# Kernel optimization log

Measured on AMD Instinct MI355X. Metric: run time of the kernel, lower is better.

Reference implementation:

```python
import jax, jax.numpy as jnp
import numpy as np

B, T, D = 1024, 512, 128  # batch, history length, embedding = num_units


def setup_inputs() -> dict:
    key = jax.random.key(0)
    ks = jax.random.split(key, 5)
    s = 1.0 / np.sqrt(2 * D)
    return {
        "rnn_input": jax.random.normal(ks[0], (B, T, D), jnp.float32),
        "att_score": jax.random.uniform(ks[1], (B, T, 1), jnp.float32),
        "gate_kernel": jax.random.normal(ks[2], (2 * D, 2 * D), jnp.float32) * s,
        "gate_bias": jnp.ones((2 * D,), jnp.float32),  # TF GRUCell init: gate bias = 1.0
        "cand_kernel": jax.random.normal(ks[3], (2 * D, D), jnp.float32) * s,
        "cand_bias": jnp.zeros((D,), jnp.float32),
        "sequence_length": jax.random.randint(ks[4], (B, 1), 1, T + 1, jnp.int32),
    }


def reference(rnn_input, att_score, gate_kernel, gate_bias, cand_kernel, cand_bias, sequence_length):
    # AUGRU (VecAttGRUCell) dynamic_rnn, return_sequence=True
    Bv, Tv, Dv = rnn_input.shape
    lens = sequence_length.reshape(Bv)                      # tf.squeeze
    x_t = jnp.transpose(rnn_input, (1, 0, 2))               # [T,B,D]
    a_t = jnp.transpose(att_score, (1, 0, 2))               # [T,B,1]
    mask = (jnp.arange(Tv)[:, None] < lens[None, :])[..., None]  # [T,B,1] bool
    h0 = jnp.zeros((Bv, Dv), rnn_input.dtype)

    def step(h, xs):
        x, a, m = xs
        gi = jnp.concatenate([x, h], -1) @ gate_kernel + gate_bias
        r, u = jnp.split(jax.nn.sigmoid(gi), 2, axis=-1)
        c = jnp.tanh(jnp.concatenate([x, r * h], -1) @ cand_kernel + cand_bias)
        u = (1.0 - a) * u                                   # attention-gated update
        new_h = u * h + (1.0 - u) * c
        h_next = jnp.where(m, new_h, h)                     # state copy-through past length
        out = jnp.where(m, new_h, 0.0)                      # dynamic_rnn zeros past length
        return h_next, out

    _, outs = jax.lax.scan(step, h0, (x_t, a_t, mask))
    return jnp.transpose(outs, (1, 0, 2))                   # [B,T,D]
```

## Files before the change

kernel.cpp:

```cpp
#include <hip/hip_runtime.h>
#include <hip/hip_bf16.h>


#define Bn 1024
#define Tn 512
#define Dn 128

typedef __attribute__((ext_vector_type(8))) short short8;
typedef __attribute__((ext_vector_type(4))) float f32x4;

#define BS 136

#define NL2E  (-1.4426950408889634f)
#define N2L2E (-2.8853900817779268f)

__device__ __forceinline__ short f2bf(float f) {
    __hip_bfloat16 h = __float2bfloat16(f);
    return __builtin_bit_cast(short, h);
}
__device__ __forceinline__ unsigned cvt_pk_bf16(float a, float b) {
    unsigned r;
    asm("v_cvt_pk_bf16_f32 %0, %1, %2" : "=v"(r) : "v"(a), "v"(b));
    return r;
}
__device__ __forceinline__ void barrier_lds() {
    __builtin_amdgcn_sched_barrier(0);
    asm volatile("s_waitcnt lgkmcnt(0)" ::: "memory");
    __builtin_amdgcn_s_barrier();
    __builtin_amdgcn_sched_barrier(0);
}

#define MFMA_(a, b, c) __builtin_amdgcn_mfma_f32_16x16x32_bf16((a), (b), (c), 0, 0, 0)

__launch_bounds__(512, 1)
__global__ void augru_kernel(const float* __restrict__ X,
                             const float* __restrict__ ATT,
                             const float* __restrict__ GK,
                             const float* __restrict__ GB,
                             const float* __restrict__ CK,
                             const float* __restrict__ CB,
                             const int*   __restrict__ SL,
                             float* __restrict__ OUT) {
    __shared__ short hb [16 * BS];
    __shared__ short rhb[16 * BS];
    __shared__ short xb [2][16 * BS];
    __shared__ float abuf[2][16];
    __shared__ int   lenbuf[16];

    const int tid  = threadIdx.x;
    const int wid  = tid >> 6;
    const int lane = tid & 63;
    const int lm   = lane & 15;
    const int q    = lane >> 4;
    const int b0   = blockIdx.x * 16;
    const int ccol = 16 * wid + lm;

    short8 fgx0[4], fgx1[4], fgh0[4], fgh1[4], fcx[4], fch[4];
#pragma unroll
    for (int ks = 0; ks < 4; ++ks) {
        short8 v0, v1, v2, v3, v4, v5;
#pragma unroll
        for (int j = 0; j < 8; ++j) {
            const int k = ks * 32 + q * 8 + j;
            v0[j] = f2bf(GK[k * 256 + ccol]);
            v1[j] = f2bf(GK[k * 256 + 128 + ccol]);
            v2[j] = f2bf(GK[(128 + k) * 256 + ccol]);
            v3[j] = f2bf(GK[(128 + k) * 256 + 128 + ccol]);
            v4[j] = f2bf(CK[k * 128 + ccol]);
            v5[j] = f2bf(CK[(128 + k) * 128 + ccol]);
        }
        fgx0[ks] = v0; fgx1[ks] = v1; fgh0[ks] = v2; fgh1[ks] = v3;
        fcx[ks] = v4;  fch[ks] = v5;
    }
    const float pb0 = GB[ccol]       * NL2E;
    const float pb1 = GB[128 + ccol] * NL2E;
    const float cbp = CB[ccol]       * N2L2E;

    for (int i = tid; i < 16 * BS; i += 512) hb[i] = 0;
    if (tid < 16) {
        lenbuf[tid]  = SL[b0 + tid];
        abuf[0][tid] = ATT[(size_t)(b0 + tid) * Tn];
    }
    const int prow = tid >> 5;
    const int pcol = (tid & 31) * 4;
    {
        float4 v = *(const float4*)(X + ((size_t)(b0 + prow) * Tn + 0) * Dn + pcol);
        uint2 pp; pp.x = cvt_pk_bf16(v.x, v.y); pp.y = cvt_pk_bf16(v.z, v.w);
        *(uint2*)&xb[0][prow * BS + pcol] = pp;
    }
    __syncthreads();

    int len_i[4];
    float h_reg[4] = {0.f, 0.f, 0.f, 0.f};
#pragma unroll
    for (int i = 0; i < 4; ++i) len_i[i] = lenbuf[q * 4 + i];

    f32x4 gxA0 = {0,0,0,0}, gxA1 = {0,0,0,0}, cxA = {0,0,0,0};
    f32x4 gxB0, gxB1, cxB;
    {
        short8 ax0[4];
#pragma unroll
        for (int ks = 0; ks < 4; ++ks)
            ax0[ks] = *(const short8*)&xb[0][lm * BS + ks * 32 + q * 8];
#pragma unroll
        for (int ks = 0; ks < 4; ++ks) {
            gxA0 = MFMA_(ax0[ks], fgx0[ks], gxA0);
            gxA1 = MFMA_(ax0[ks], fgx1[ks], gxA1);
            cxA  = MFMA_(ax0[ks], fcx[ks],  cxA);
        }
        float4 v = *(const float4*)(X + ((size_t)(b0 + prow) * Tn + 1) * Dn + pcol);
        uint2 pp; pp.x = cvt_pk_bf16(v.x, v.y); pp.y = cvt_pk_bf16(v.z, v.w);
        *(uint2*)&xb[1][prow * BS + pcol] = pp;
    }
    __syncthreads();

#define STEP_BODY(t, GIN0, GIN1, CIN, GOUT0, GOUT1, COUT)                         \
    {                                                                             \
        const int cur = (t) & 1, nxt = cur ^ 1;                                   \
        const int tp1 = ((t) + 1 < Tn) ? (t) + 1 : Tn - 1;                        \
        const int tp2 = ((t) + 2 < Tn) ? (t) + 2 : Tn - 1;                        \
        float4 xpre = *(const float4*)(X + ((size_t)(b0 + prow) * Tn + tp2) * Dn + pcol); \
        float  apre = (tid < 16) ? ATT[(size_t)(b0 + tid) * Tn + tp1] : 0.0f;     \
                                  \
        short8 axn[4], ah[4];                                                     \
        _Pragma("unroll")                                                         \
        for (int ks = 0; ks < 4; ++ks) {                                          \
            axn[ks] = *(const short8*)&xb[nxt][lm * BS + ks * 32 + q * 8];        \
            ah[ks]  = *(const short8*)&hb[lm * BS + ks * 32 + q * 8];             \
        }                                                                         \
         \
        f32x4 g0 = GIN0, g1 = GIN1;                                               \
        f32x4 n0 = {0,0,0,0}, n1 = {0,0,0,0}, n2 = {0,0,0,0};                     \
        _Pragma("unroll")                                                         \
        for (int ks = 0; ks < 4; ++ks) {                                          \
            g0 = MFMA_(ah[ks], fgh0[ks], g0);                                     \
            g1 = MFMA_(ah[ks], fgh1[ks], g1);                                     \
        }                                                                         \
        _Pragma("unroll")                                                         \
        for (int ks = 0; ks < 4; ++ks) {                                          \
            n0 = MFMA_(axn[ks], fgx0[ks], n0);                                    \
            n1 = MFMA_(axn[ks], fgx1[ks], n1);                                    \
            n2 = MFMA_(axn[ks], fcx[ks],  n2);                                    \
        }                                                                         \
              \
        float am[4], up[4], rhv[4];                                               \
        _Pragma("unroll")                                                         \
        for (int i = 0; i < 4; ++i) am[i] = 1.0f - abuf[cur][q * 4 + i];          \
        _Pragma("unroll")                                                         \
        for (int i = 0; i < 4; ++i) {                                             \
            const float e0 = __builtin_amdgcn_exp2f(fmaf(g0[i], NL2E, pb0));      \
            rhv[i] = __builtin_amdgcn_rcpf(1.0f + e0) * h_reg[i];                 \
            const float e1 = __builtin_amdgcn_exp2f(fmaf(g1[i], NL2E, pb1));      \
            up[i] = am[i] * __builtin_amdgcn_rcpf(1.0f + e1);                     \
        }                                                                         \
        {                                                                         \
            const unsigned pA_ = cvt_pk_bf16(rhv[0], rhv[1]);                     \
            const unsigned pB_ = cvt_pk_bf16(rhv[2], rhv[3]);                     \
            rhb[(q * 4 + 0) * BS + ccol] = (short)pA_;                            \
            rhb[(q * 4 + 1) * BS + ccol] = (short)(pA_ >> 16);                    \
            rhb[(q * 4 + 2) * BS + ccol] = (short)pB_;                            \
            rhb[(q * 4 + 3) * BS + ccol] = (short)(pB_ >> 16);                    \
        }                                                                         \
        barrier_lds();                                                            \
                               \
        f32x4 cc = CIN;                                                           \
        _Pragma("unroll")                                                         \
        for (int ks = 0; ks < 4; ++ks) {                                          \
            short8 arh = *(const short8*)&rhb[lm * BS + ks * 32 + q * 8];         \
            cc = MFMA_(arh, fch[ks], cc);                                         \
        }                                                                         \
                             \
        float hxv[4];                                                             \
        _Pragma("unroll")                                                         \
        for (int i = 0; i < 4; ++i) {                                             \
            const int row = q * 4 + i;                                            \
            const float e  = __builtin_amdgcn_exp2f(fmaf(cc[i], N2L2E, cbp));     \
            const float cv = fmaf(2.0f, __builtin_amdgcn_rcpf(1.0f + e), -1.0f);  \
            const float hn = fmaf(up[i], h_reg[i] - cv, cv);                      \
            const bool valid = ((t) < len_i[i]);                                  \
            const float hnext = valid ? hn : h_reg[i];                            \
            OUT[((size_t)(b0 + row) * Tn + (t)) * Dn + ccol] = valid ? hn : 0.0f; \
            h_reg[i] = hnext;                                                     \
            hxv[i] = hnext;                                                       \
        }                                                                         \
        {                                                                         \
            const unsigned pA_ = cvt_pk_bf16(hxv[0], hxv[1]);                     \
            const unsigned pB_ = cvt_pk_bf16(hxv[2], hxv[3]);                     \
            hb[(q * 4 + 0) * BS + ccol] = (short)pA_;                             \
            hb[(q * 4 + 1) * BS + ccol] = (short)(pA_ >> 16);                     \
            hb[(q * 4 + 2) * BS + ccol] = (short)pB_;                             \
            hb[(q * 4 + 3) * BS + ccol] = (short)(pB_ >> 16);                     \
        }                                                                         \
                            \
        {                                                                         \
            uint2 pp_;                                                            \
            pp_.x = cvt_pk_bf16(xpre.x, xpre.y);                                  \
            pp_.y = cvt_pk_bf16(xpre.z, xpre.w);                                  \
            *(uint2*)&xb[cur][prow * BS + pcol] = pp_;                            \
            if (tid < 16) abuf[nxt][tid] = apre;                                  \
        }                                                                         \
        barrier_lds();                                                            \
        GOUT0 = n0; GOUT1 = n1; COUT = n2;                                        \
    }

    for (int t = 0; t < Tn; t += 2) {
        STEP_BODY(t,     gxA0, gxA1, cxA, gxB0, gxB1, cxB)
        STEP_BODY(t + 1, gxB0, gxB1, cxB, gxA0, gxA1, cxA)
    }
#undef STEP_BODY
}

extern "C" void kernel_launch(void* const* d_in, const int* in_sizes, int n_in,
                              void* d_out, int out_size, void* d_ws, size_t ws_size,
                              hipStream_t stream) {
    (void)in_sizes; (void)n_in; (void)d_ws; (void)ws_size; (void)out_size;
    const float* X   = (const float*)d_in[0];
    const float* ATT = (const float*)d_in[1];
    const float* GK  = (const float*)d_in[2];
    const float* GB  = (const float*)d_in[3];
    const float* CK  = (const float*)d_in[4];
    const float* CB  = (const float*)d_in[5];
    const int*   SL  = (const int*)d_in[6];
    float* OUT = (float*)d_out;

    augru_kernel<<<dim3(Bn / 16), dim3(512), 0, stream>>>(X, ATT, GK, GB, CK, CB, SL, OUT);
}
```

Baseline: 526.6 us.

## Halve waves per block, giving each wave two column tiles of the GRU step

Each block now runs 4 waves instead of 8, and each wave computes two 16-column slices. It holds twice the bf16 weight fragments in registers and interleaves two independent MFMA accumulation chains. This is meant to cut barrier participants and improve MFMA issue overlap within a wave. The cost is a longer serial per-wave MFMA and transcendental sequence per timestep and much higher register pressure. X staging now uses 8-wide loads per thread, and the staged x for the next step is re-read inside a macro rather than taken from the early prefetch registers. That may expose global load latency unless the compiler merges the duplicate loads.

```diff
diff --git a/kernel.cpp b/kernel.cpp
--- a/kernel.cpp
+++ b/kernel.cpp
@@ -8,6 +8,7 @@
 
 typedef __attribute__((ext_vector_type(8))) short short8;
 typedef __attribute__((ext_vector_type(4))) float f32x4;
+typedef __attribute__((ext_vector_type(4))) unsigned uint4v;
 
 #define BS 136
 
@@ -32,7 +33,7 @@
 
 #define MFMA_(a, b, c) __builtin_amdgcn_mfma_f32_16x16x32_bf16((a), (b), (c), 0, 0, 0)
 
-__launch_bounds__(512, 1)
+__launch_bounds__(256, 1)
 __global__ void augru_kernel(const float* __restrict__ X,
                              const float* __restrict__ ATT,
                              const float* __restrict__ GK,
@@ -53,64 +54,77 @@
     const int lm   = lane & 15;
     const int q    = lane >> 4;
     const int b0   = blockIdx.x * 16;
-    const int ccol = 16 * wid + lm;
-
-    short8 fgx0[4], fgx1[4], fgh0[4], fgh1[4], fcx[4], fch[4];
-#pragma unroll
-    for (int ks = 0; ks < 4; ++ks) {
-        short8 v0, v1, v2, v3, v4, v5;
-#pragma unroll
-        for (int j = 0; j < 8; ++j) {
-            const int k = ks * 32 + q * 8 + j;
-            v0[j] = f2bf(GK[k * 256 + ccol]);
-            v1[j] = f2bf(GK[k * 256 + 128 + ccol]);
-            v2[j] = f2bf(GK[(128 + k) * 256 + ccol]);
-            v3[j] = f2bf(GK[(128 + k) * 256 + 128 + ccol]);
-            v4[j] = f2bf(CK[k * 128 + ccol]);
-            v5[j] = f2bf(CK[(128 + k) * 128 + ccol]);
+
+    const int colBase = 32 * wid + lm;
+
+    short8 fgx0[2][4], fgx1[2][4], fgh0[2][4], fgh1[2][4], fcx[2][4], fch[2][4];
+    float pb0[2], pb1[2], cbp[2];
+#pragma unroll
+    for (int s = 0; s < 2; ++s) {
+        const int c = colBase + 16 * s;
+#pragma unroll
+        for (int ks = 0; ks < 4; ++ks) {
+            short8 v0, v1, v2, v3, v4, v5;
+#pragma unroll
+            for (int j = 0; j < 8; ++j) {
+                const int k = ks * 32 + q * 8 + j;
+                v0[j] = f2bf(GK[k * 256 + c]);
+                v1[j] = f2bf(GK[k * 256 + 128 + c]);
+                v2[j] = f2bf(GK[(128 + k) * 256 + c]);
+                v3[j] = f2bf(GK[(128 + k) * 256 + 128 + c]);
+                v4[j] = f2bf(CK[k * 128 + c]);
+                v5[j] = f2bf(CK[(128 + k) * 128 + c]);
+            }
+            fgx0[s][ks] = v0; fgx1[s][ks] = v1;
+            fgh0[s][ks] = v2; fgh1[s][ks] = v3;
+            fcx[s][ks] = v4;  fch[s][ks] = v5;
         }
-        fgx0[ks] = v0; fgx1[ks] = v1; fgh0[ks] = v2; fgh1[ks] = v3;
-        fcx[ks] = v4;  fch[ks] = v5;
-    }
-    const float pb0 = GB[ccol]       * NL2E;
-    const float pb1 = GB[128 + ccol] * NL2E;
-    const float cbp = CB[ccol]       * N2L2E;
-
-    for (int i = tid; i < 16 * BS; i += 512) hb[i] = 0;
+        pb0[s] = GB[c]       * NL2E;
+        pb1[s] = GB[128 + c] * NL2E;
+        cbp[s] = CB[c]       * N2L2E;
+    }
+
+    for (int i = tid; i < 16 * BS; i += 256) hb[i] = 0;
     if (tid < 16) {
         lenbuf[tid]  = SL[b0 + tid];
         abuf[0][tid] = ATT[(size_t)(b0 + tid) * Tn];
     }
-    const int prow = tid >> 5;
-    const int pcol = (tid & 31) * 4;
-    {
-        float4 v = *(const float4*)(X + ((size_t)(b0 + prow) * Tn + 0) * Dn + pcol);
-        uint2 pp; pp.x = cvt_pk_bf16(v.x, v.y); pp.y = cvt_pk_bf16(v.z, v.w);
-        *(uint2*)&xb[0][prow * BS + pcol] = pp;
-    }
+    const int prow = tid >> 4;
+    const int pc8  = (tid & 15) * 8;
+#define STAGE_X(slot, tt) {                                                        \
+        const float* xp_ = X + ((size_t)(b0 + prow) * Tn + (tt)) * Dn + pc8;       \
+        float4 a_ = *(const float4*)xp_;                                           \
+        float4 b_ = *(const float4*)(xp_ + 4);                                     \
+        uint4v pp_;                                                                \
+        pp_[0] = cvt_pk_bf16(a_.x, a_.y); pp_[1] = cvt_pk_bf16(a_.z, a_.w);        \
+        pp_[2] = cvt_pk_bf16(b_.x, b_.y); pp_[3] = cvt_pk_bf16(b_.z, b_.w);        \
+        *(uint4v*)&xb[slot][prow * BS + pc8] = pp_; }
+
+    STAGE_X(0, 0)
     __syncthreads();
 
     int len_i[4];
-    float h_reg[4] = {0.f, 0.f, 0.f, 0.f};
+    float h_reg[2][4] = {{0.f,0.f,0.f,0.f},{0.f,0.f,0.f,0.f}};
 #pragma unroll
     for (int i = 0; i < 4; ++i) len_i[i] = lenbuf[q * 4 + i];
 
-    f32x4 gxA0 = {0,0,0,0}, gxA1 = {0,0,0,0}, cxA = {0,0,0,0};
-    f32x4 gxB0, gxB1, cxB;
+    f32x4 gx0A[2], gx1A[2], cxA[2], gx0B[2], gx1B[2], cxB[2];
+#pragma unroll
+    for (int s = 0; s < 2; ++s) { gx0A[s] = (f32x4){0,0,0,0}; gx1A[s] = (f32x4){0,0,0,0}; cxA[s] = (f32x4){0,0,0,0}; }
     {
         short8 ax0[4];
 #pragma unroll
         for (int ks = 0; ks < 4; ++ks)
             ax0[ks] = *(const short8*)&xb[0][lm * BS + ks * 32 + q * 8];
 #pragma unroll
-        for (int ks = 0; ks < 4; ++ks) {
-            gxA0 = MFMA_(ax0[ks], fgx0[ks], gxA0);
-            gxA1 = MFMA_(ax0[ks], fgx1[ks], gxA1);
-            cxA  = MFMA_(ax0[ks], fcx[ks],  cxA);
-        }
-        float4 v = *(const float4*)(X + ((size_t)(b0 + prow) * Tn + 1) * Dn + pcol);
-        uint2 pp; pp.x = cvt_pk_bf16(v.x, v.y); pp.y = cvt_pk_bf16(v.z, v.w);
-        *(uint2*)&xb[1][prow * BS + pcol] = pp;
+        for (int ks = 0; ks < 4; ++ks)
+#pragma unroll
+            for (int s = 0; s < 2; ++s) {
+                gx0A[s] = MFMA_(ax0[ks], fgx0[s][ks], gx0A[s]);
+                gx1A[s] = MFMA_(ax0[ks], fgx1[s][ks], gx1A[s]);
+                cxA[s]  = MFMA_(ax0[ks], fcx[s][ks],  cxA[s]);
+            }
+        STAGE_X(1, 1)
     }
     __syncthreads();
 
@@ -119,95 +133,114 @@
         const int cur = (t) & 1, nxt = cur ^ 1;                                   \
         const int tp1 = ((t) + 1 < Tn) ? (t) + 1 : Tn - 1;                        \
         const int tp2 = ((t) + 2 < Tn) ? (t) + 2 : Tn - 1;                        \
-        float4 xpre = *(const float4*)(X + ((size_t)(b0 + prow) * Tn + tp2) * Dn + pcol); \
+        const float* xp = X + ((size_t)(b0 + prow) * Tn + tp2) * Dn + pc8;        \
+        float4 xpre0 = *(const float4*)xp;                                        \
+        float4 xpre1 = *(const float4*)(xp + 4);                                  \
         float  apre = (tid < 16) ? ATT[(size_t)(b0 + tid) * Tn + tp1] : 0.0f;     \
-                                  \
+                     \
         short8 axn[4], ah[4];                                                     \
         _Pragma("unroll")                                                         \
         for (int ks = 0; ks < 4; ++ks) {                                          \
             axn[ks] = *(const short8*)&xb[nxt][lm * BS + ks * 32 + q * 8];        \
             ah[ks]  = *(const short8*)&hb[lm * BS + ks * 32 + q * 8];             \
         }                                                                         \
-         \
-        f32x4 g0 = GIN0, g1 = GIN1;                                               \
-        f32x4 n0 = {0,0,0,0}, n1 = {0,0,0,0}, n2 = {0,0,0,0};                     \
-        _Pragma("unroll")                                                         \
-        for (int ks = 0; ks < 4; ++ks) {                                          \
-            g0 = MFMA_(ah[ks], fgh0[ks], g0);                                     \
-            g1 = MFMA_(ah[ks], fgh1[ks], g1);                                     \
-        }                                                                         \
-        _Pragma("unroll")                                                         \
-        for (int ks = 0; ks < 4; ++ks) {                                          \
-            n0 = MFMA_(axn[ks], fgx0[ks], n0);                                    \
-            n1 = MFMA_(axn[ks], fgx1[ks], n1);                                    \
-            n2 = MFMA_(axn[ks], fcx[ks],  n2);                                    \
-        }                                                                         \
-              \
-        float am[4], up[4], rhv[4];                                               \
+             \
+        f32x4 g0[2], g1[2], n0[2], n1[2], n2[2];                                  \
+        _Pragma("unroll")                                                         \
+        for (int s = 0; s < 2; ++s) {                                             \
+            g0[s] = GIN0[s]; g1[s] = GIN1[s];                                     \
+            n0[s] = (f32x4){0,0,0,0}; n1[s] = (f32x4){0,0,0,0}; n2[s] = (f32x4){0,0,0,0}; \
+        }                                                                         \
+        _Pragma("unroll")                                                         \
+        for (int ks = 0; ks < 4; ++ks)                                            \
+            _Pragma("unroll")                                                     \
+            for (int s = 0; s < 2; ++s) {                                         \
+                g0[s] = MFMA_(ah[ks], fgh0[s][ks], g0[s]);                        \
+                g1[s] = MFMA_(ah[ks], fgh1[s][ks], g1[s]);                        \
+            }                                                                     \
+        _Pragma("unroll")                                                         \
+        for (int ks = 0; ks < 4; ++ks)                                            \
+            _Pragma("unroll")                                                     \
+            for (int s = 0; s < 2; ++s) {                                         \
+                n0[s] = MFMA_(axn[ks], fgx0[s][ks], n0[s]);                       \
+                n1[s] = MFMA_(axn[ks], fgx1[s][ks], n1[s]);                       \
+                n2[s] = MFMA_(axn[ks], fcx[s][ks],  n2[s]);                       \
+            }                                                                     \
+               \
+        float am[4], up[2][4];                                                    \
         _Pragma("unroll")                                                         \
         for (int i = 0; i < 4; ++i) am[i] = 1.0f - abuf[cur][q * 4 + i];          \
         _Pragma("unroll")                                                         \
-        for (int i = 0; i < 4; ++i) {                                             \
-            const float e0 = __builtin_amdgcn_exp2f(fmaf(g0[i], NL2E, pb0));      \
-            rhv[i] = __builtin_amdgcn_rcpf(1.0f + e0) * h_reg[i];                 \
-            const float e1 = __builtin_amdgcn_exp2f(fmaf(g1[i], NL2E, pb1));      \
-            up[i] = am[i] * __builtin_amdgcn_rcpf(1.0f + e1);                     \
-        }                                                                         \
-        {                                                                         \
+        for (int s = 0; s < 2; ++s) {                                             \
+            float rhv[4];                                                         \
+            _Pragma("unroll")                                                     \
+            for (int i = 0; i < 4; ++i) {                                         \
+                const float e0 = __builtin_amdgcn_exp2f(fmaf(g0[s][i], NL2E, pb0[s])); \
+                rhv[i] = __builtin_amdgcn_rcpf(1.0f + e0) * h_reg[s][i];          \
+                const float e1 = __builtin_amdgcn_exp2f(fmaf(g1[s][i], NL2E, pb1[s])); \
+                up[s][i] = am[i] * __builtin_amdgcn_rcpf(1.0f + e1);              \
+            }                                                                     \
             const unsigned pA_ = cvt_pk_bf16(rhv[0], rhv[1]);                     \
             const unsigned pB_ = cvt_pk_bf16(rhv[2], rhv[3]);                     \
-            rhb[(q * 4 + 0) * BS + ccol] = (short)pA_;                            \
-            rhb[(q * 4 + 1) * BS + ccol] = (short)(pA_ >> 16);                    \
-            rhb[(q * 4 + 2) * BS + ccol] = (short)pB_;                            \
-            rhb[(q * 4 + 3) * BS + ccol] = (short)(pB_ >> 16);                    \
+            const int c_ = colBase + 16 * s;                                      \
+            rhb[(q * 4 + 0) * BS + c_] = (short)pA_;                              \
+            rhb[(q * 4 + 1) * BS + c_] = (short)(pA_ >> 16);                      \
+            rhb[(q * 4 + 2) * BS + c_] = (short)pB_;                              \
+            rhb[(q * 4 + 3) * BS + c_] = (short)(pB_ >> 16);                      \
         }                                                                         \
         barrier_lds();                                                            \
-                               \
-        f32x4 cc = CIN;                                                           \
-        _Pragma("unroll")                                                         \
-        for (int ks = 0; ks < 4; ++ks) {                                          \
-            short8 arh = *(const short8*)&rhb[lm * BS + ks * 32 + q * 8];         \
-            cc = MFMA_(arh, fch[ks], cc);                                         \
-        }                                                                         \
-                             \
-        float hxv[4];                                                             \
-        _Pragma("unroll")                                                         \
-        for (int i = 0; i < 4; ++i) {                                             \
-            const int row = q * 4 + i;                                            \
-            const float e  = __builtin_amdgcn_exp2f(fmaf(cc[i], N2L2E, cbp));     \
-            const float cv = fmaf(2.0f, __builtin_amdgcn_rcpf(1.0f + e), -1.0f);  \
-            const float hn = fmaf(up[i], h_reg[i] - cv, cv);                      \
-            const bool valid = ((t) < len_i[i]);                                  \
-            const float hnext = valid ? hn : h_reg[i];                            \
-            OUT[((size_t)(b0 + row) * Tn + (t)) * Dn + ccol] = valid ? hn : 0.0f; \
-            h_reg[i] = hnext;                                                     \
-            hxv[i] = hnext;                                                       \
-        }                                                                         \
-        {                                                                         \
+                                        \
+        short8 arh[4];                                                            \
+        _Pragma("unroll")                                                         \
+        for (int ks = 0; ks < 4; ++ks)                                            \
+            arh[ks] = *(const short8*)&rhb[lm * BS + ks * 32 + q * 8];            \
+        f32x4 cc[2];                                                              \
+        _Pragma("unroll")                                                         \
+        for (int s = 0; s < 2; ++s) cc[s] = CIN[s];                               \
+        _Pragma("unroll")                                                         \
+        for (int ks = 0; ks < 4; ++ks)                                            \
+            _Pragma("unroll")                                                     \
+            for (int s = 0; s < 2; ++s)                                           \
+                cc[s] = MFMA_(arh[ks], fch[s][ks], cc[s]);                        \
+                                          \
+        _Pragma("unroll")                                                         \
+        for (int s = 0; s < 2; ++s) {                                             \
+            float hxv[4];                                                         \
+            const int c_ = colBase + 16 * s;                                      \
+            _Pragma("unroll")                                                     \
+            for (int i = 0; i < 4; ++i) {                                         \
+                const int row = q * 4 + i;                                        \
+                const float e  = __builtin_amdgcn_exp2f(fmaf(cc[s][i], N2L2E, cbp[s])); \
+                const float cv = fmaf(2.0f, __builtin_amdgcn_rcpf(1.0f + e), -1.0f); \
+                const float hn = fmaf(up[s][i], h_reg[s][i] - cv, cv);            \
+                const bool valid = ((t) < len_i[i]);                              \
+                const float hnext = valid ? hn : h_reg[s][i];                     \
+                OUT[((size_t)(b0 + row) * Tn + (t)) * Dn + c_] = valid ? hn : 0.0f; \
+                h_reg[s][i] = hnext;                                              \
+                hxv[i] = hnext;                                                   \
+            }                                                                     \
             const unsigned pA_ = cvt_pk_bf16(hxv[0], hxv[1]);                     \
             const unsigned pB_ = cvt_pk_bf16(hxv[2], hxv[3]);                     \
-            hb[(q * 4 + 0) * BS + ccol] = (short)pA_;                             \
-            hb[(q * 4 + 1) * BS + ccol] = (short)(pA_ >> 16);                     \
-            hb[(q * 4 + 2) * BS + ccol] = (short)pB_;                             \
-            hb[(q * 4 + 3) * BS + ccol] = (short)(pB_ >> 16);                     \
+            hb[(q * 4 + 0) * BS + c_] = (short)pA_;                               \
+            hb[(q * 4 + 1) * BS + c_] = (short)(pA_ >> 16);                       \
+            hb[(q * 4 + 2) * BS + c_] = (short)pB_;                               \
+            hb[(q * 4 + 3) * BS + c_] = (short)(pB_ >> 16);                       \
         }                                                                         \
                             \
-        {                                                                         \
-            uint2 pp_;                                                            \
-            pp_.x = cvt_pk_bf16(xpre.x, xpre.y);                                  \
-            pp_.y = cvt_pk_bf16(xpre.z, xpre.w);                                  \
-            *(uint2*)&xb[cur][prow * BS + pcol] = pp_;                            \
-            if (tid < 16) abuf[nxt][tid] = apre;                                  \
-        }                                                                         \
+        STAGE_X(cur, tp2)                                                         \
+        if (tid < 16) abuf[nxt][tid] = apre;                                      \
+        (void)xpre0; (void)xpre1;                                                 \
         barrier_lds();                                                            \
-        GOUT0 = n0; GOUT1 = n1; COUT = n2;                                        \
+        _Pragma("unroll")                                                         \
+        for (int s = 0; s < 2; ++s) { GOUT0[s] = n0[s]; GOUT1[s] = n1[s]; COUT[s] = n2[s]; } \
     }
 
     for (int t = 0; t < Tn; t += 2) {
-        STEP_BODY(t,     gxA0, gxA1, cxA, gxB0, gxB1, cxB)
-        STEP_BODY(t + 1, gxB0, gxB1, cxB, gxA0, gxA1, cxA)
+        STEP_BODY(t,     gx0A, gx1A, cxA, gx0B, gx1B, cxB)
+        STEP_BODY(t + 1, gx0B, gx1B, cxB, gx0A, gx1A, cxA)
     }
 #undef STEP_BODY
+#undef STAGE_X
 }
 
 extern "C" void kernel_launch(void* const* d_in, const int* in_sizes, int n_in,
@@ -223,5 +256,5 @@
     const int*   SL  = (const int*)d_in[6];
     float* OUT = (float*)d_out;
 
-    augru_kernel<<<dim3(Bn / 16), dim3(512), 0, stream>>>(X, ATT, GK, GB, CK, CB, SL, OUT);
-}
+    augru_kernel<<<dim3(Bn / 16), dim3(256), 0, stream>>>(X, ATT, GK, GB, CK, CB, SL, OUT);
+}
```

Measured after the change: 892.4 us. +69.5%, slower.

## Swap MFMA operands so each lane owns a batch row and four contiguous columns

Applied to the files above, without the earlier changes.

The MFMA A/B operands are swapped so the accumulator is transposed: each lane now holds four consecutive hidden units for a single batch row instead of one unit across four rows. This lets h and r*h be written to LDS as one 8-byte packed store instead of four scalar short stores, and the output as one 16-byte float4 global store instead of four strided scalar stores. The attention scale and length mask become one value per lane, while the biases become per-register arrays. It aims to cut LDS store instructions and uncoalesced global writes on the serial recurrence path, at the cost of a few extra registers.

```diff
diff --git a/kernel.cpp b/kernel.cpp
--- a/kernel.cpp
+++ b/kernel.cpp
@@ -53,7 +53,9 @@
     const int lm   = lane & 15;
     const int q    = lane >> 4;
     const int b0   = blockIdx.x * 16;
-    const int ccol = 16 * wid + lm;
+    const int cb   = 16 * wid;
+    const int ccol = cb + lm;
+    const int c0   = cb + 4 * q;
 
     short8 fgx0[4], fgx1[4], fgh0[4], fgh1[4], fcx[4], fch[4];
 #pragma unroll
@@ -72,9 +74,13 @@
         fgx0[ks] = v0; fgx1[ks] = v1; fgh0[ks] = v2; fgh1[ks] = v3;
         fcx[ks] = v4;  fch[ks] = v5;
     }
-    const float pb0 = GB[ccol]       * NL2E;
-    const float pb1 = GB[128 + ccol] * NL2E;
-    const float cbp = CB[ccol]       * N2L2E;
+    float pb0[4], pb1[4], cbp[4];
+#pragma unroll
+    for (int i = 0; i < 4; ++i) {
+        pb0[i] = GB[c0 + i]       * NL2E;
+        pb1[i] = GB[128 + c0 + i] * NL2E;
+        cbp[i] = CB[c0 + i]       * N2L2E;
+    }
 
     for (int i = tid; i < 16 * BS; i += 512) hb[i] = 0;
     if (tid < 16) {
@@ -90,10 +96,8 @@
     }
     __syncthreads();
 
-    int len_i[4];
+    const int lenr = lenbuf[lm];
     float h_reg[4] = {0.f, 0.f, 0.f, 0.f};
-#pragma unroll
-    for (int i = 0; i < 4; ++i) len_i[i] = lenbuf[q * 4 + i];
 
     f32x4 gxA0 = {0,0,0,0}, gxA1 = {0,0,0,0}, cxA = {0,0,0,0};
     f32x4 gxB0, gxB1, cxB;
@@ -104,9 +108,9 @@
             ax0[ks] = *(const short8*)&xb[0][lm * BS + ks * 32 + q * 8];
 #pragma unroll
         for (int ks = 0; ks < 4; ++ks) {
-            gxA0 = MFMA_(ax0[ks], fgx0[ks], gxA0);
-            gxA1 = MFMA_(ax0[ks], fgx1[ks], gxA1);
-            cxA  = MFMA_(ax0[ks], fcx[ks],  cxA);
+            gxA0 = MFMA_(fgx0[ks], ax0[ks], gxA0);
+            gxA1 = MFMA_(fgx1[ks], ax0[ks], gxA1);
+            cxA  = MFMA_(fcx[ks],  ax0[ks], cxA);
         }
         float4 v = *(const float4*)(X + ((size_t)(b0 + prow) * Tn + 1) * Dn + pcol);
         uint2 pp; pp.x = cvt_pk_bf16(v.x, v.y); pp.y = cvt_pk_bf16(v.z, v.w);
@@ -121,75 +125,68 @@
         const int tp2 = ((t) + 2 < Tn) ? (t) + 2 : Tn - 1;                        \
         float4 xpre = *(const float4*)(X + ((size_t)(b0 + prow) * Tn + tp2) * Dn + pcol); \
         float  apre = (tid < 16) ? ATT[(size_t)(b0 + tid) * Tn + tp1] : 0.0f;     \
-                                  \
+                      \
         short8 axn[4], ah[4];                                                     \
         _Pragma("unroll")                                                         \
         for (int ks = 0; ks < 4; ++ks) {                                          \
             axn[ks] = *(const short8*)&xb[nxt][lm * BS + ks * 32 + q * 8];        \
             ah[ks]  = *(const short8*)&hb[lm * BS + ks * 32 + q * 8];             \
         }                                                                         \
-         \
+             \
         f32x4 g0 = GIN0, g1 = GIN1;                                               \
         f32x4 n0 = {0,0,0,0}, n1 = {0,0,0,0}, n2 = {0,0,0,0};                     \
         _Pragma("unroll")                                                         \
         for (int ks = 0; ks < 4; ++ks) {                                          \
-            g0 = MFMA_(ah[ks], fgh0[ks], g0);                                     \
-            g1 = MFMA_(ah[ks], fgh1[ks], g1);                                     \
-        }                                                                         \
-        _Pragma("unroll")                                                         \
-        for (int ks = 0; ks < 4; ++ks) {                                          \
-            n0 = MFMA_(axn[ks], fgx0[ks], n0);                                    \
-            n1 = MFMA_(axn[ks], fgx1[ks], n1);                                    \
-            n2 = MFMA_(axn[ks], fcx[ks],  n2);                                    \
-        }                                                                         \
-              \
-        float am[4], up[4], rhv[4];                                               \
-        _Pragma("unroll")                                                         \
-        for (int i = 0; i < 4; ++i) am[i] = 1.0f - abuf[cur][q * 4 + i];          \
+            g0 = MFMA_(fgh0[ks], ah[ks], g0);                                     \
+            g1 = MFMA_(fgh1[ks], ah[ks], g1);                                     \
+        }                                                                         \
+        _Pragma("unroll")                                                         \
+        for (int ks = 0; ks < 4; ++ks) {                                          \
+            n0 = MFMA_(fgx0[ks], axn[ks], n0);                                    \
+            n1 = MFMA_(fgx1[ks], axn[ks], n1);                                    \
+            n2 = MFMA_(fcx[ks],  axn[ks], n2);                                    \
+        }                                                                         \
+            \
+        const float am_ = 1.0f - abuf[cur][lm];                                   \
+        float up[4], rhv[4];                                                      \
         _Pragma("unroll")                                                         \
         for (int i = 0; i < 4; ++i) {                                             \
-            const float e0 = __builtin_amdgcn_exp2f(fmaf(g0[i], NL2E, pb0));      \
+            const float e0 = __builtin_amdgcn_exp2f(fmaf(g0[i], NL2E, pb0[i]));   \
             rhv[i] = __builtin_amdgcn_rcpf(1.0f + e0) * h_reg[i];                 \
-            const float e1 = __builtin_amdgcn_exp2f(fmaf(g1[i], NL2E, pb1));      \
-            up[i] = am[i] * __builtin_amdgcn_rcpf(1.0f + e1);                     \
-        }                                                                         \
-        {                                                                         \
-            const unsigned pA_ = cvt_pk_bf16(rhv[0], rhv[1]);                     \
-            const unsigned pB_ = cvt_pk_bf16(rhv[2], rhv[3]);                     \
-            rhb[(q * 4 + 0) * BS + ccol] = (short)pA_;                            \
-            rhb[(q * 4 + 1) * BS + ccol] = (short)(pA_ >> 16);                    \
-            rhb[(q * 4 + 2) * BS + ccol] = (short)pB_;                            \
-            rhb[(q * 4 + 3) * BS + ccol] = (short)(pB_ >> 16);                    \
+            const float e1 = __builtin_amdgcn_exp2f(fmaf(g1[i], NL2E, pb1[i]));   \
+            up[i] = am_ * __builtin_amdgcn_rcpf(1.0f + e1);                       \
+        }                                                                         \
+        {                           \
+            uint2 rp;                                                             \
+            rp.x = cvt_pk_bf16(rhv[0], rhv[1]);                                   \
+            rp.y = cvt_pk_bf16(rhv[2], rhv[3]);                                   \
+            *(uint2*)&rhb[lm * BS + c0] = rp;                                     \
         }                                                                         \
         barrier_lds();                                                            \
-                               \
+                                        \
         f32x4 cc = CIN;                                                           \
         _Pragma("unroll")                                                         \
         for (int ks = 0; ks < 4; ++ks) {                                          \
             short8 arh = *(const short8*)&rhb[lm * BS + ks * 32 + q * 8];         \
-            cc = MFMA_(arh, fch[ks], cc);                                         \
-        }                                                                         \
-                             \
-        float hxv[4];                                                             \
+            cc = MFMA_(fch[ks], arh, cc);                                         \
+        }                                                                         \
+                       \
+        const bool valid = ((t) < lenr);                                          \
+        f32x4 outv;                                                               \
         _Pragma("unroll")                                                         \
         for (int i = 0; i < 4; ++i) {                                             \
-            const int row = q * 4 + i;                                            \
-            const float e  = __builtin_amdgcn_exp2f(fmaf(cc[i], N2L2E, cbp));     \
+            const float e  = __builtin_amdgcn_exp2f(fmaf(cc[i], N2L2E, cbp[i]));  \
             const float cv = fmaf(2.0f, __builtin_amdgcn_rcpf(1.0f + e), -1.0f);  \
             const float hn = fmaf(up[i], h_reg[i] - cv, cv);                      \
-            const bool valid = ((t) < len_i[i]);                                  \
-            const float hnext = valid ? hn : h_reg[i];                            \
-            OUT[((size_t)(b0 + row) * Tn + (t)) * Dn + ccol] = valid ? hn : 0.0f; \
-            h_reg[i] = hnext;                                                     \
-            hxv[i] = hnext;                                                       \
-        }                                                                         \
-        {                                                                         \
-            const unsigned pA_ = cvt_pk_bf16(hxv[0], hxv[1]);                     \
-            const unsigned pB_ = cvt_pk_bf16(hxv[2], hxv[3]);                     \
-            hb[(q * 4 + 0) * BS + ccol] = (short)pA_;                             \
-            hb[(q * 4 + 1) * BS + ccol] = (short)(pA_ >> 16);                     \
-            hb[(q * 4 + 2) * BS + ccol] = (short)pB_;                             \
-            hb[(q * 4 + 3) * BS + ccol] = (short)(pB_ >> 16);                     \
+            h_reg[i] = valid ? hn : h_reg[i];                                     \
+            outv[i]  = valid ? hn : 0.0f;                                         \
+        }                                                                         \
+        *(f32x4*)(OUT + ((size_t)(b0 + lm) * Tn + (t)) * Dn + c0) = outv;         \
+        {                            \
+            uint2 hp;                                                             \
+            hp.x = cvt_pk_bf16(h_reg[0], h_reg[1]);                               \
+            hp.y = cvt_pk_bf16(h_reg[2], h_reg[3]);                               \
+            *(uint2*)&hb[lm * BS + c0] = hp;                                      \
         }                                                                         \
                             \
         {                                                                         \
```

After: 536.0 us. No clear change (+1.8%).

## Move next-step input projection MFMAs after gate barrier and relax final barrier wait

Applied to the files above, without the earlier changes.

The twelve MFMAs that project the next timestep's input are moved out of the gate phase. They now sit after the first barrier, next to the candidate MFMAs, so the recurrent chain (h load, gate MFMA, sigmoid, r*h store, barrier) carries less work. The reset-scaled hidden and next-x LDS fragments are loaded in one batch. The final barrier now waits with lgkmcnt(1) instead of lgkmcnt(0), which risks an LDS write not having landed before other waves read it. Smaller changes store 1-att directly in LDS and replace per-step output address math with incrementing offsets.

```diff
diff --git a/kernel.cpp b/kernel.cpp
--- a/kernel.cpp
+++ b/kernel.cpp
@@ -26,6 +26,12 @@
 __device__ __forceinline__ void barrier_lds() {
     __builtin_amdgcn_sched_barrier(0);
     asm volatile("s_waitcnt lgkmcnt(0)" ::: "memory");
+    __builtin_amdgcn_s_barrier();
+    __builtin_amdgcn_sched_barrier(0);
+}
+__device__ __forceinline__ void barrier_lds_c1() {
+    __builtin_amdgcn_sched_barrier(0);
+    asm volatile("s_waitcnt lgkmcnt(1)" ::: "memory");
     __builtin_amdgcn_s_barrier();
     __builtin_amdgcn_sched_barrier(0);
 }
@@ -79,7 +85,7 @@
     for (int i = tid; i < 16 * BS; i += 512) hb[i] = 0;
     if (tid < 16) {
         lenbuf[tid]  = SL[b0 + tid];
-        abuf[0][tid] = ATT[(size_t)(b0 + tid) * Tn];
+        abuf[0][tid] = 1.0f - ATT[(size_t)(b0 + tid) * Tn];
     }
     const int prow = tid >> 5;
     const int pcol = (tid & 31) * 4;
@@ -92,8 +98,12 @@
 
     int len_i[4];
     float h_reg[4] = {0.f, 0.f, 0.f, 0.f};
-#pragma unroll
-    for (int i = 0; i < 4; ++i) len_i[i] = lenbuf[q * 4 + i];
+    unsigned out_off[4];
+#pragma unroll
+    for (int i = 0; i < 4; ++i) {
+        len_i[i]   = lenbuf[q * 4 + i];
+        out_off[i] = (unsigned)(((b0 + q * 4 + i) * Tn) * Dn + ccol);
+    }
 
     f32x4 gxA0 = {0,0,0,0}, gxA1 = {0,0,0,0}, cxA = {0,0,0,0};
     f32x4 gxB0, gxB1, cxB;
@@ -121,31 +131,21 @@
         const int tp2 = ((t) + 2 < Tn) ? (t) + 2 : Tn - 1;                        \
         float4 xpre = *(const float4*)(X + ((size_t)(b0 + prow) * Tn + tp2) * Dn + pcol); \
         float  apre = (tid < 16) ? ATT[(size_t)(b0 + tid) * Tn + tp1] : 0.0f;     \
-                                  \
-        short8 axn[4], ah[4];                                                     \
-        _Pragma("unroll")                                                         \
-        for (int ks = 0; ks < 4; ++ks) {                                          \
-            axn[ks] = *(const short8*)&xb[nxt][lm * BS + ks * 32 + q * 8];        \
-            ah[ks]  = *(const short8*)&hb[lm * BS + ks * 32 + q * 8];             \
-        }                                                                         \
-         \
+              \
+        short8 ah[4];                                                             \
+        _Pragma("unroll")                                                         \
+        for (int ks = 0; ks < 4; ++ks)                                            \
+            ah[ks] = *(const short8*)&hb[lm * BS + ks * 32 + q * 8];              \
         f32x4 g0 = GIN0, g1 = GIN1;                                               \
-        f32x4 n0 = {0,0,0,0}, n1 = {0,0,0,0}, n2 = {0,0,0,0};                     \
         _Pragma("unroll")                                                         \
         for (int ks = 0; ks < 4; ++ks) {                                          \
             g0 = MFMA_(ah[ks], fgh0[ks], g0);                                     \
             g1 = MFMA_(ah[ks], fgh1[ks], g1);                                     \
         }                                                                         \
-        _Pragma("unroll")                                                         \
-        for (int ks = 0; ks < 4; ++ks) {                                          \
-            n0 = MFMA_(axn[ks], fgx0[ks], n0);                                    \
-            n1 = MFMA_(axn[ks], fgx1[ks], n1);                                    \
-            n2 = MFMA_(axn[ks], fcx[ks],  n2);                                    \
-        }                                                                         \
               \
         float am[4], up[4], rhv[4];                                               \
         _Pragma("unroll")                                                         \
-        for (int i = 0; i < 4; ++i) am[i] = 1.0f - abuf[cur][q * 4 + i];          \
+        for (int i = 0; i < 4; ++i) am[i] = abuf[cur][q * 4 + i];      \
         _Pragma("unroll")                                                         \
         for (int i = 0; i < 4; ++i) {                                             \
             const float e0 = __builtin_amdgcn_exp2f(fmaf(g0[i], NL2E, pb0));      \
@@ -162,24 +162,35 @@
             rhb[(q * 4 + 3) * BS + ccol] = (short)(pB_ >> 16);                    \
         }                                                                         \
         barrier_lds();                                                            \
-                               \
+         \
+        short8 arh[4], axn[4];                                                    \
+        _Pragma("unroll")                                                         \
+        for (int ks = 0; ks < 4; ++ks) {                                          \
+            arh[ks] = *(const short8*)&rhb[lm * BS + ks * 32 + q * 8];            \
+            axn[ks] = *(const short8*)&xb[nxt][lm * BS + ks * 32 + q * 8];        \
+        }                                                                         \
         f32x4 cc = CIN;                                                           \
         _Pragma("unroll")                                                         \
+        for (int ks = 0; ks < 4; ++ks)                                            \
+            cc = MFMA_(arh[ks], fch[ks], cc);                                     \
+        f32x4 n0 = {0,0,0,0}, n1 = {0,0,0,0}, n2 = {0,0,0,0};                     \
+        _Pragma("unroll")                                                         \
         for (int ks = 0; ks < 4; ++ks) {                                          \
-            short8 arh = *(const short8*)&rhb[lm * BS + ks * 32 + q * 8];         \
-            cc = MFMA_(arh, fch[ks], cc);                                         \
-        }                                                                         \
-                             \
+            n0 = MFMA_(axn[ks], fgx0[ks], n0);                                    \
+            n1 = MFMA_(axn[ks], fgx1[ks], n1);                                    \
+            n2 = MFMA_(axn[ks], fcx[ks],  n2);                                    \
+        }                                                                         \
+                     \
         float hxv[4];                                                             \
         _Pragma("unroll")                                                         \
         for (int i = 0; i < 4; ++i) {                                             \
-            const int row = q * 4 + i;                                            \
             const float e  = __builtin_amdgcn_exp2f(fmaf(cc[i], N2L2E, cbp));     \
             const float cv = fmaf(2.0f, __builtin_amdgcn_rcpf(1.0f + e), -1.0f);  \
             const float hn = fmaf(up[i], h_reg[i] - cv, cv);                      \
             const bool valid = ((t) < len_i[i]);                                  \
             const float hnext = valid ? hn : h_reg[i];                            \
-            OUT[((size_t)(b0 + row) * Tn + (t)) * Dn + ccol] = valid ? hn : 0.0f; \
+            OUT[out_off[i]] = valid ? hn : 0.0f;                                  \
+            out_off[i] += Dn;                                                     \
             h_reg[i] = hnext;                                                     \
             hxv[i] = hnext;                                                       \
         }                                                                         \
@@ -191,15 +202,16 @@
             hb[(q * 4 + 2) * BS + ccol] = (short)pB_;                             \
             hb[(q * 4 + 3) * BS + ccol] = (short)(pB_ >> 16);                     \
         }                                                                         \
-                            \
+             \
+             \
         {                                                                         \
             uint2 pp_;                                                            \
             pp_.x = cvt_pk_bf16(xpre.x, xpre.y);                                  \
             pp_.y = cvt_pk_bf16(xpre.z, xpre.w);                                  \
             *(uint2*)&xb[cur][prow * BS + pcol] = pp_;                            \
-            if (tid < 16) abuf[nxt][tid] = apre;                                  \
-        }                                                                         \
-        barrier_lds();                                                            \
+            if (tid < 16) abuf[nxt][tid] = 1.0f - apre;                           \
+        }                                                                         \
+        barrier_lds_c1();                                                         \
         GOUT0 = n0; GOUT1 = n1; COUT = n2;                                        \
     }
 
```

New measurement: 574.5 us. 9.1% more time.
